# Optimization experiments

Hardware: AMD Instinct MI355X
Metric: run time of the kernel (lower is better)

The kernel has to match this reference:

```python
import jax, jax.numpy as jnp
import numpy as np

D_MODEL = 256
N_HEADS = 8


def setup_inputs() -> dict:
    key = jax.random.key(0)
    ks = jax.random.split(key, 12)
    B, S, d, H = 4, 1024, D_MODEL, N_HEADS
    s = 0.02
    return {
        "Q": jax.random.normal(ks[0], (B, S, d), jnp.float32),
        "K": jax.random.normal(ks[1], (B, S, d), jnp.float32),
        "V": jax.random.normal(ks[2], (B, S, d), jnp.float32),
        "Wq": jax.random.normal(ks[3], (d, d * H), jnp.float32) * s,
        "bq": jnp.zeros((d * H,), jnp.float32),
        "Wk": jax.random.normal(ks[4], (d, d * H), jnp.float32) * s,
        "bk": jnp.zeros((d * H,), jnp.float32),
        "Wv": jax.random.normal(ks[5], (d, d * H), jnp.float32) * s,
        "bv": jnp.zeros((d * H,), jnp.float32),
        "Wo": jax.random.normal(ks[6], (H * d, d), jnp.float32) * s,
        "bo": jnp.zeros((d,), jnp.float32),
    }


def reference(Q, K, V, Wq, bq, Wk, bk, Wv, bv, Wo, bo):
    B, S, d = Q.shape
    H = N_HEADS
    # projections: [B,S,d] -> [B,S,H*d] -> [B,H,S,d] (head_dim == d_model here)
    q = (Q @ Wq + bq).reshape(B, S, H, d).transpose(0, 2, 1, 3)
    k = (K @ Wk + bk).reshape(B, S, H, d).transpose(0, 2, 1, 3)
    v = (V @ Wv + bv).reshape(B, S, H, d).transpose(0, 2, 1, 3)
    scores = jnp.einsum("bhqd,bhkd->bhqk", q, k) / jnp.sqrt(jnp.float32(d))
    attn = jax.nn.softmax(scores, axis=-1)
    out = jnp.einsum("bhqk,bhkd->bhqd", attn, v)  # [B,H,S,d]
    out = out.transpose(0, 2, 1, 3).reshape(B, S, H * d)
    return out @ Wo + bo
```

## Files before the change

kernel.cpp:

```cpp
#include <hip/hip_runtime.h>
#include <stdint.h>

#define NB 4
#define SEQ 1024
#define DM 256
#define NH 8

typedef __attribute__((ext_vector_type(8))) short bf8;
typedef __attribute__((ext_vector_type(4))) float f4;

__device__ __forceinline__ unsigned short f2bf(float f) {
  union { float f; uint32_t u; } c; c.f = f;
  uint32_t u = c.u;
  return (unsigned short)((u + 0x7FFFu + ((u >> 16) & 1u)) >> 16);
}

__device__ __forceinline__ void gl_lds16(const unsigned short* g, short* l) {
  __builtin_amdgcn_global_load_lds(
      (const __attribute__((address_space(1))) unsigned int*)g,
      (__attribute__((address_space(3))) unsigned int*)l, 16, 0, 0);
}


__global__ __launch_bounds__(256) void prep_kernel(
    const float* __restrict__ Wq, const float* __restrict__ Wk,
    const float* __restrict__ Wv, const float* __restrict__ Wo,
    const float* __restrict__ Q, const float* __restrict__ K,
    const float* __restrict__ V,
    unsigned short* __restrict__ Wt3, unsigned short* __restrict__ WoT,
    unsigned short* __restrict__ Xbf) {
  const int z = blockIdx.y;
  const int tid = threadIdx.x;
  if (z >= 4) {
    const float* src = (z == 4) ? Q : (z == 5) ? K : V;
    const size_t off = (size_t)blockIdx.x * 1024 + tid * 4;
    const float4 v = *(const float4*)(src + off);
    short4 s;
    s.x = (short)f2bf(v.x); s.y = (short)f2bf(v.y);
    s.z = (short)f2bf(v.z); s.w = (short)f2bf(v.w);
    *(short4*)(Xbf + (size_t)(z - 4) * 4096 * 256 + off) = s;
    return;
  }
  if (blockIdx.x >= 512) return;
  const float* in;
  unsigned short* out;
  int R, C, bx, by;
  if (z < 3) {
    in = (z == 0) ? Wq : (z == 1) ? Wk : Wv;
    out = Wt3 + (size_t)z * 2048 * 256;
    R = 256; C = 2048; bx = blockIdx.x & 63; by = blockIdx.x >> 6;
  } else {
    in = Wo; out = WoT;
    R = 2048; C = 256; bx = blockIdx.x & 7; by = blockIdx.x >> 3;
  }
  __shared__ float t[32][33];
  const int c0 = bx * 32, r0 = by * 32;
  const int tx = tid & 31, ty = tid >> 5;
#pragma unroll
  for (int i = 0; i < 4; i++) {
    int r = r0 + ty + i * 8;
    t[ty + i * 8][tx] = in[(size_t)r * C + c0 + tx];
  }
  __syncthreads();
#pragma unroll
  for (int i = 0; i < 4; i++) {
    int c = c0 + ty + i * 8;
    out[(size_t)c * R + r0 + tx] = f2bf(t[tx][ty + i * 8]);
  }
}

__global__ __launch_bounds__(256) void proj_kernel(
    const unsigned short* __restrict__ Xbf, const unsigned short* __restrict__ Wt3,
    const float* __restrict__ bq, const float* __restrict__ bk, const float* __restrict__ bv,
    unsigned short* __restrict__ q_frag, unsigned short* __restrict__ k_frag,
    unsigned short* __restrict__ v_frag) {
  const int z = blockIdx.z;
  const unsigned short* X = Xbf + (size_t)z * 4096 * 256;
  const unsigned short* Wt = Wt3 + (size_t)z * 2048 * 256;
  const float* bias = (z == 0) ? bq : (z == 1) ? bk : bv;

  __shared__ short a_lds[128 * 32];
  __shared__ short b_lds[128 * 32];

  const int tid = threadIdx.x;
  const int wid = tid >> 6, lane = tid & 63;
  const int quad = lane >> 4, l16 = lane & 15;
  const int wm = wid >> 1, wn = wid & 1;
  const int m0 = blockIdx.x * 128, n0 = blockIdx.y * 128;

  f4 acc[4][4];
  const f4 z4 = {0.f, 0.f, 0.f, 0.f};
#pragma unroll
  for (int i = 0; i < 4; i++)
#pragma unroll
    for (int j = 0; j < 4; j++) acc[i][j] = z4;

  const int srow = lane >> 2;
  const int schunk = lane & 3;
  const int cxor = quad ^ (l16 & 3);

  for (int ko = 0; ko < 8; ko++) {
    const int k0 = ko * 32;
#pragma unroll
    for (int j = 0; j < 2; j++) {
      const int i = wid * 2 + j;
      const int row = i * 16 + srow;
      const int sc = (schunk ^ (row & 3)) * 8;
      gl_lds16(X + (size_t)(m0 + row) * DM + k0 + sc, a_lds + i * 512);
      gl_lds16(Wt + (size_t)(n0 + row) * DM + k0 + sc, b_lds + i * 512);
    }
    __syncthreads();
    bf8 af[4], bfv[4];
#pragma unroll
    for (int mi = 0; mi < 4; mi++)
      af[mi] = *(const bf8*)(a_lds + (wm * 64 + mi * 16 + l16) * 32 + cxor * 8);
#pragma unroll
    for (int ni = 0; ni < 4; ni++)
      bfv[ni] = *(const bf8*)(b_lds + (wn * 64 + ni * 16 + l16) * 32 + cxor * 8);
    if (z < 2) {
#pragma unroll
      for (int ni = 0; ni < 4; ni++)
#pragma unroll
        for (int mi = 0; mi < 4; mi++)
          acc[ni][mi] = __builtin_amdgcn_mfma_f32_16x16x32_bf16(bfv[ni], af[mi], acc[ni][mi], 0, 0, 0);
    } else {
#pragma unroll
      for (int mi = 0; mi < 4; mi++)
#pragma unroll
        for (int ni = 0; ni < 4; ni++)
          acc[mi][ni] = __builtin_amdgcn_mfma_f32_16x16x32_bf16(af[mi], bfv[ni], acc[mi][ni], 0, 0, 0);
    }
    __syncthreads();
  }

  if (z < 2) {
    const float scale = (z == 0) ? 0.0901684400f : 1.0f;
    unsigned short* dst = (z == 0) ? q_frag : k_frag;
#pragma unroll
    for (int ni = 0; ni < 4; ni++) {
      const int nb = n0 + wn * 64 + ni * 16 + quad * 4;
      const float4 b4 = *(const float4*)(bias + nb);
      const int h = nb >> 8, dd = nb & 255;
      const int dq = (dd >> 3) & 3, jh = dd & 7;
#pragma unroll
      for (int mi = 0; mi < 4; mi++) {
        const int tok = m0 + wm * 64 + mi * 16 + l16;
        const int b = tok >> 10, sr = tok & 1023;
        const size_t idx = ((size_t)(b * NH + h) * 64 + (sr >> 4)) * 4096 +
                           (size_t)(dd >> 5) * 512 + ((sr & 15) + 16 * dq) * 8 + jh;
        short4 s4;
        s4.x = (short)f2bf((acc[ni][mi][0] + b4.x) * scale);
        s4.y = (short)f2bf((acc[ni][mi][1] + b4.y) * scale);
        s4.z = (short)f2bf((acc[ni][mi][2] + b4.z) * scale);
        s4.w = (short)f2bf((acc[ni][mi][3] + b4.w) * scale);
        *(short4*)(dst + idx) = s4;
      }
    }
  } else {
#pragma unroll
    for (int ni = 0; ni < 4; ni++) {
      const int n = n0 + wn * 64 + ni * 16 + l16;
      const float bsv = bias[n];
      const int h = n >> 8, d = n & 255;
#pragma unroll
      for (int mi = 0; mi < 4; mi++) {
        const int m = m0 + wm * 64 + mi * 16 + quad * 4;
        const int b = m >> 10, sr = m & 1023;
        const size_t idx = ((size_t)(b * NH + h) * 16 + (d >> 4)) * 16384 +
                           (size_t)(sr >> 5) * 512 +
                           ((d & 15) + 16 * ((sr >> 3) & 3)) * 8 + (sr & 7);
        short4 s4;
        s4.x = (short)f2bf(acc[mi][ni][0] + bsv);
        s4.y = (short)f2bf(acc[mi][ni][1] + bsv);
        s4.z = (short)f2bf(acc[mi][ni][2] + bsv);
        s4.w = (short)f2bf(acc[mi][ni][3] + bsv);
        *(short4*)(v_frag + idx) = s4;
      }
    }
  }
}

__global__ __launch_bounds__(256, 2) void attn_kernel(
    const unsigned short* __restrict__ q_frag, const unsigned short* __restrict__ k_frag,
    const unsigned short* __restrict__ v_frag, unsigned short* __restrict__ o_ws) {
  __shared__ short k_lds[3 * 8192];
  __shared__ short p_lds[2][2][64][40];
  __shared__ float l_sh[2][64];

  const int tid = threadIdx.x;
  const int wid = tid >> 6, lane = tid & 63;
  const int quad = lane >> 4, l16 = lane & 15;
  const int wq = wid >> 1, wk = wid & 1;
  const int blk = blockIdx.x;
  const int g = blk & 7;
  const int qt = (blk >> 3) & 15;
  const int bh = g + 8 * (blk >> 7);
  const size_t fbase = (size_t)bh * 262144;

  const unsigned short* ksrc = k_frag + fbase + (size_t)wid * 2048 + lane * 8;
#pragma unroll
  for (int jj = 0; jj < 4; jj++) {
    gl_lds16(ksrc + jj * 512, &k_lds[wid * 2048 + jj * 512]);
    gl_lds16(ksrc + 8192 + jj * 512, &k_lds[2 * 8192 + wid * 2048 + jj * 512]);
  }

  bf8 qf[2][8];
#pragma unroll
  for (int qi = 0; qi < 2; qi++) {
    const unsigned short* qp =
        q_frag + fbase + (size_t)(qt * 4 + wq * 2 + qi) * 4096 + lane * 8;
#pragma unroll
    for (int c = 0; c < 8; c++) qf[qi][c] = *(const bf8*)(qp + c * 512);
  }

  const f4 z4 = {0.f, 0.f, 0.f, 0.f};
  f4 Oacc[4][4];
#pragma unroll
  for (int i = 0; i < 4; i++)
#pragma unroll
    for (int j = 0; j < 4; j++) Oacc[i][j] = z4;
  float lpart[2][4] = {{0.f, 0.f, 0.f, 0.f}, {0.f, 0.f, 0.f, 0.f}};

  __syncthreads();

  bf8 vpre[8];
  const unsigned short* vsrc = v_frag + fbase + (size_t)(wid * 4) * 16384 + lane * 8;

  for (int t = 0; t < 16; t++) {
    const int cur = t & 1;
    if (t < 15) {
      const unsigned short* s0 = ksrc + (size_t)(t + 1) * 16384;
#pragma unroll
      for (int jj = 0; jj < 4; jj++)
        gl_lds16(s0 + jj * 512, &k_lds[(cur ^ 1) * 8192 + wid * 2048 + jj * 512]);
    }
    const short* kb_base = &k_lds[(wk ? 2 : cur) * 8192];
    f4 S00 = z4, S01 = z4, S10 = z4, S11 = z4;
#pragma unroll
    for (int c = 0; c < 8; c++) {
      const bf8 kb0 = *(const bf8*)(kb_base + c * 512 + lane * 8);
      const bf8 kb1 = *(const bf8*)(kb_base + 4096 + c * 512 + lane * 8);
      S00 = __builtin_amdgcn_mfma_f32_16x16x32_bf16(qf[0][c], kb0, S00, 0, 0, 0);
      S01 = __builtin_amdgcn_mfma_f32_16x16x32_bf16(qf[0][c], kb1, S01, 0, 0, 0);
      S10 = __builtin_amdgcn_mfma_f32_16x16x32_bf16(qf[1][c], kb0, S10, 0, 0, 0);
      S11 = __builtin_amdgcn_mfma_f32_16x16x32_bf16(qf[1][c], kb1, S11, 0, 0, 0);
    }
    __syncthreads();
    if (t < 15) {
      const unsigned short* s1 = ksrc + (size_t)(t + 1) * 16384 + 8192;
#pragma unroll
      for (int jj = 0; jj < 4; jj++)
        gl_lds16(s1 + jj * 512, &k_lds[2 * 8192 + wid * 2048 + jj * 512]);
    }
    if (t > 0) {
      const int prv = cur ^ 1;
#pragma unroll
      for (int ks = 0; ks < 2; ks++) {
        bf8 pb[4];
#pragma unroll
        for (int nq = 0; nq < 4; nq++)
          pb[nq] = *(const bf8*)(&p_lds[prv][ks][nq * 16 + l16][quad * 8]);
#pragma unroll
        for (int mi = 0; mi < 4; mi++)
#pragma unroll
          for (int nq = 0; nq < 4; nq++)
            Oacc[mi][nq] = __builtin_amdgcn_mfma_f32_16x16x32_bf16(
                vpre[ks * 4 + mi], pb[nq], Oacc[mi][nq], 0, 0, 0);
      }
    }
#pragma unroll
    for (int ks = 0; ks < 2; ks++)
#pragma unroll
      for (int mi = 0; mi < 4; mi++)
        vpre[ks * 4 + mi] =
            *(const bf8*)(vsrc + (size_t)mi * 16384 + (size_t)(2 * t + ks) * 512);
#pragma unroll
    for (int reg = 0; reg < 4; reg++) {
      {
        const int qrow = wq * 32 + quad * 4 + reg;
        const float p0 = exp2f(S00[reg]);
        const float p1 = exp2f(S01[reg]);
        lpart[0][reg] += p0 + p1;
        union { float f; uint32_t u; } c0, c1;
        c0.f = p0; c1.f = p1;
        p_lds[cur][wk][qrow][l16] = (short)((c0.u + 0x8000u) >> 16);
        p_lds[cur][wk][qrow][16 + l16] = (short)((c1.u + 0x8000u) >> 16);
      }
      {
        const int qrow = wq * 32 + 16 + quad * 4 + reg;
        const float p0 = exp2f(S10[reg]);
        const float p1 = exp2f(S11[reg]);
        lpart[1][reg] += p0 + p1;
        union { float f; uint32_t u; } c0, c1;
        c0.f = p0; c1.f = p1;
        p_lds[cur][wk][qrow][l16] = (short)((c0.u + 0x8000u) >> 16);
        p_lds[cur][wk][qrow][16 + l16] = (short)((c1.u + 0x8000u) >> 16);
      }
    }
    __syncthreads();
  }

  {
#pragma unroll
    for (int ks = 0; ks < 2; ks++) {
      bf8 pb[4];
#pragma unroll
      for (int nq = 0; nq < 4; nq++)
        pb[nq] = *(const bf8*)(&p_lds[1][ks][nq * 16 + l16][quad * 8]);
#pragma unroll
      for (int mi = 0; mi < 4; mi++)
#pragma unroll
        for (int nq = 0; nq < 4; nq++)
          Oacc[mi][nq] = __builtin_amdgcn_mfma_f32_16x16x32_bf16(
              vpre[ks * 4 + mi], pb[nq], Oacc[mi][nq], 0, 0, 0);
    }
  }

#pragma unroll
  for (int qi = 0; qi < 2; qi++)
#pragma unroll
    for (int reg = 0; reg < 4; reg++) {
      float v = lpart[qi][reg];
      v += __shfl_xor(v, 1, 64);
      v += __shfl_xor(v, 2, 64);
      v += __shfl_xor(v, 4, 64);
      v += __shfl_xor(v, 8, 64);
      if (l16 == 0) l_sh[wk][wq * 32 + qi * 16 + quad * 4 + reg] = v;
    }
  __syncthreads();

  const int b = bh >> 3, h = bh & 7;
#pragma unroll
  for (int nq = 0; nq < 4; nq++) {
    const int q = nq * 16 + l16;
    const float inv = 1.f / (l_sh[0][q] + l_sh[1][q]);
    const size_t base = ((size_t)b * SEQ + qt * 64 + q) * (NH * DM) + h * DM + wid * 64;
#pragma unroll
    for (int mi = 0; mi < 4; mi++) {
      short4 s4;
      s4.x = (short)f2bf(Oacc[mi][nq][0] * inv);
      s4.y = (short)f2bf(Oacc[mi][nq][1] * inv);
      s4.z = (short)f2bf(Oacc[mi][nq][2] * inv);
      s4.w = (short)f2bf(Oacc[mi][nq][3] * inv);
      *(short4*)(o_ws + base + mi * 16 + quad * 4) = s4;
    }
  }
}

__global__ __launch_bounds__(256) void outproj_kernel(
    const unsigned short* __restrict__ o_ws, const unsigned short* __restrict__ WoT,
    const float* __restrict__ bo, float* __restrict__ out) {
  __shared__ short a_lds[32][136];
  __shared__ short b_lds[64][136];

  const int tid = threadIdx.x;
  const int wid = tid >> 6, lane = tid & 63;
  const int quad = lane >> 4, l16 = lane & 15;
  const int wm = wid & 1, wn = wid >> 1;
  const int m0 = blockIdx.x * 32, n0 = blockIdx.y * 64;

  const f4 z4 = {0.f, 0.f, 0.f, 0.f};
  f4 acc[2];
#pragma unroll
  for (int i = 0; i < 2; i++) acc[i] = z4;

  const int ch = tid & 15, row = tid >> 4;
  for (int ko = 0; ko < 16; ko++) {
    const int k0 = ko * 128;
#pragma unroll
    for (int rb = 0; rb < 2; rb++) {
      int r = row + rb * 16;
      *(bf8*)(&a_lds[r][ch * 8]) = *(const bf8*)(o_ws + (size_t)(m0 + r) * 2048 + k0 + ch * 8);
    }
#pragma unroll
    for (int rb = 0; rb < 4; rb++) {
      int r = row + rb * 16;
      *(bf8*)(&b_lds[r][ch * 8]) = *(const bf8*)(WoT + (size_t)(n0 + r) * 2048 + k0 + ch * 8);
    }
    __syncthreads();
#pragma unroll
    for (int kc = 0; kc < 4; kc++) {
      const bf8 af = *(const bf8*)(&a_lds[wm * 16 + l16][kc * 32 + quad * 8]);
      bf8 bfv[2];
#pragma unroll
      for (int ni = 0; ni < 2; ni++)
        bfv[ni] = *(const bf8*)(&b_lds[wn * 32 + ni * 16 + l16][kc * 32 + quad * 8]);
#pragma unroll
      for (int ni = 0; ni < 2; ni++)
        acc[ni] = __builtin_amdgcn_mfma_f32_16x16x32_bf16(af, bfv[ni], acc[ni], 0, 0, 0);
    }
    __syncthreads();
  }
#pragma unroll
  for (int ni = 0; ni < 2; ni++) {
    const int n = n0 + wn * 32 + ni * 16 + l16;
    const float bv = bo[n];
#pragma unroll
    for (int reg = 0; reg < 4; reg++) {
      const int m = m0 + wm * 16 + quad * 4 + reg;
      out[(size_t)m * DM + n] = acc[ni][reg] + bv;
    }
  }
}

extern "C" void kernel_launch(void* const* d_in, const int* in_sizes, int n_in,
                              void* d_out, int out_size, void* d_ws, size_t ws_size,
                              hipStream_t stream) {
  const float* Q  = (const float*)d_in[0];
  const float* K  = (const float*)d_in[1];
  const float* V  = (const float*)d_in[2];
  const float* Wq = (const float*)d_in[3];
  const float* bq = (const float*)d_in[4];
  const float* Wk = (const float*)d_in[5];
  const float* bk = (const float*)d_in[6];
  const float* Wv = (const float*)d_in[7];
  const float* bv = (const float*)d_in[8];
  const float* Wo = (const float*)d_in[9];
  const float* bo = (const float*)d_in[10];
  float* out = (float*)d_out;

  char* ws = (char*)d_ws;
  const size_t QS = (size_t)NB * NH * SEQ * DM * 2;
  unsigned short* q_frag = (unsigned short*)(ws);
  unsigned short* k_frag = (unsigned short*)(ws + QS);
  unsigned short* v_frag = (unsigned short*)(ws + 2 * QS);
  unsigned short* o_ws   = (unsigned short*)(ws + 3 * QS);
  const size_t WT = (size_t)2048 * 256 * 2;
  unsigned short* Wt3 = (unsigned short*)(ws + 4 * QS);
  unsigned short* WoT = (unsigned short*)(ws + 4 * QS + 3 * WT);
  unsigned short* Xbf = o_ws;

  prep_kernel<<<dim3(1024, 7), 256, 0, stream>>>(Wq, Wk, Wv, Wo, Q, K, V,
                                                 Wt3, WoT, Xbf);
  proj_kernel<<<dim3(32, 16, 3), 256, 0, stream>>>(Xbf, Wt3, bq, bk, bv,
                                                   q_frag, k_frag, v_frag);
  attn_kernel<<<512, 256, 0, stream>>>(q_frag, k_frag, v_frag, o_ws);
  outproj_kernel<<<dim3(128, 4), 256, 0, stream>>>(o_ws, WoT, bo, out);
}
```

Before: 171.0 us.

## Restructure attention loop to 32-key tiles with triple-buffered K prefetch

The attention main loop now processes 32-key tiles in 32 iterations instead of 64-key tiles in 16. Each wave owns 16 query rows across all keys rather than splitting keys between wave pairs, which removes the second row-sum buffer and the split P layout. K tiles rotate through a three-slot LDS ring with a two-ahead prefetch, and the two syncthreads per iteration become one explicit lgkmcnt wait plus barrier, with scheduling fences. The intent is less synchronisation and better overlap of loads with MFMA work. In exchange there are more iterations, each with less MFMA work and smaller register fragments, and the code depends on exact buffer index arithmetic.

Result: no change. 174.0 us (+1.8%).

```diff
diff --git a/kernel.cpp b/kernel.cpp
--- a/kernel.cpp
+++ b/kernel.cpp
@@ -184,33 +184,30 @@
     const unsigned short* __restrict__ q_frag, const unsigned short* __restrict__ k_frag,
     const unsigned short* __restrict__ v_frag, unsigned short* __restrict__ o_ws) {
   __shared__ short k_lds[3 * 8192];
-  __shared__ short p_lds[2][2][64][40];
-  __shared__ float l_sh[2][64];
+  __shared__ short p_lds[2][64][40];
+  __shared__ float l_sh[64];
 
   const int tid = threadIdx.x;
   const int wid = tid >> 6, lane = tid & 63;
   const int quad = lane >> 4, l16 = lane & 15;
-  const int wq = wid >> 1, wk = wid & 1;
   const int blk = blockIdx.x;
   const int g = blk & 7;
   const int qt = (blk >> 3) & 15;
   const int bh = g + 8 * (blk >> 7);
   const size_t fbase = (size_t)bh * 262144;
 
-  const unsigned short* ksrc = k_frag + fbase + (size_t)wid * 2048 + lane * 8;
+  const unsigned short* kdma_src = k_frag + fbase + (size_t)wid * 2048 + lane * 8;
 #pragma unroll
   for (int jj = 0; jj < 4; jj++) {
-    gl_lds16(ksrc + jj * 512, &k_lds[wid * 2048 + jj * 512]);
-    gl_lds16(ksrc + 8192 + jj * 512, &k_lds[2 * 8192 + wid * 2048 + jj * 512]);
-  }
-
-  bf8 qf[2][8];
-#pragma unroll
-  for (int qi = 0; qi < 2; qi++) {
-    const unsigned short* qp =
-        q_frag + fbase + (size_t)(qt * 4 + wq * 2 + qi) * 4096 + lane * 8;
-#pragma unroll
-    for (int c = 0; c < 8; c++) qf[qi][c] = *(const bf8*)(qp + c * 512);
+    gl_lds16(kdma_src + jj * 512, &k_lds[wid * 2048 + jj * 512]);
+    gl_lds16(kdma_src + 8192 + jj * 512, &k_lds[8192 + wid * 2048 + jj * 512]);
+  }
+
+  bf8 qf[8];
+  {
+    const unsigned short* qp = q_frag + fbase + (size_t)(qt * 4 + wid) * 4096 + lane * 8;
+#pragma unroll
+    for (int kc = 0; kc < 8; kc++) qf[kc] = *(const bf8*)(qp + kc * 512);
   }
 
   const f4 z4 = {0.f, 0.f, 0.f, 0.f};
@@ -219,121 +216,112 @@
   for (int i = 0; i < 4; i++)
 #pragma unroll
     for (int j = 0; j < 4; j++) Oacc[i][j] = z4;
-  float lpart[2][4] = {{0.f, 0.f, 0.f, 0.f}, {0.f, 0.f, 0.f, 0.f}};
+  float lpart[4] = {0.f, 0.f, 0.f, 0.f};
 
   __syncthreads();
 
-  bf8 vpre[8];
+  bf8 vpre[4];
   const unsigned short* vsrc = v_frag + fbase + (size_t)(wid * 4) * 16384 + lane * 8;
-
-  for (int t = 0; t < 16; t++) {
-    const int cur = t & 1;
-    if (t < 15) {
-      const unsigned short* s0 = ksrc + (size_t)(t + 1) * 16384;
+  short* const pB = &p_lds[0][0][0];
+
+  int kRd = 0;
+  int kPre = 2 * 8192;
+
+#pragma unroll 1
+  for (int t = 0; t < 32; ++t) {
+    if (t < 30) {
+      const unsigned short* s0 = kdma_src + (size_t)(t + 2) * 8192;
 #pragma unroll
       for (int jj = 0; jj < 4; jj++)
-        gl_lds16(s0 + jj * 512, &k_lds[(cur ^ 1) * 8192 + wid * 2048 + jj * 512]);
-    }
-    const short* kb_base = &k_lds[(wk ? 2 : cur) * 8192];
-    f4 S00 = z4, S01 = z4, S10 = z4, S11 = z4;
-#pragma unroll
-    for (int c = 0; c < 8; c++) {
-      const bf8 kb0 = *(const bf8*)(kb_base + c * 512 + lane * 8);
-      const bf8 kb1 = *(const bf8*)(kb_base + 4096 + c * 512 + lane * 8);
-      S00 = __builtin_amdgcn_mfma_f32_16x16x32_bf16(qf[0][c], kb0, S00, 0, 0, 0);
-      S01 = __builtin_amdgcn_mfma_f32_16x16x32_bf16(qf[0][c], kb1, S01, 0, 0, 0);
-      S10 = __builtin_amdgcn_mfma_f32_16x16x32_bf16(qf[1][c], kb0, S10, 0, 0, 0);
-      S11 = __builtin_amdgcn_mfma_f32_16x16x32_bf16(qf[1][c], kb1, S11, 0, 0, 0);
-    }
-    __syncthreads();
-    if (t < 15) {
-      const unsigned short* s1 = ksrc + (size_t)(t + 1) * 16384 + 8192;
-#pragma unroll
-      for (int jj = 0; jj < 4; jj++)
-        gl_lds16(s1 + jj * 512, &k_lds[2 * 8192 + wid * 2048 + jj * 512]);
-    }
+        gl_lds16(s0 + jj * 512, &k_lds[kPre + wid * 2048 + jj * 512]);
+    }
+    __builtin_amdgcn_sched_barrier(0);
+
+    f4 S0a = z4, S0b = z4, S1a = z4, S1b = z4;
+#pragma unroll
+    for (int cc = 0; cc < 4; cc++) {
+      const bf8 k0a = *(const bf8*)(&k_lds[kRd + (2 * cc) * 512 + lane * 8]);
+      const bf8 k0b = *(const bf8*)(&k_lds[kRd + (2 * cc + 1) * 512 + lane * 8]);
+      const bf8 k1a = *(const bf8*)(&k_lds[kRd + (8 + 2 * cc) * 512 + lane * 8]);
+      const bf8 k1b = *(const bf8*)(&k_lds[kRd + (8 + 2 * cc + 1) * 512 + lane * 8]);
+      S0a = __builtin_amdgcn_mfma_f32_16x16x32_bf16(qf[2 * cc], k0a, S0a, 0, 0, 0);
+      S0b = __builtin_amdgcn_mfma_f32_16x16x32_bf16(qf[2 * cc + 1], k0b, S0b, 0, 0, 0);
+      S1a = __builtin_amdgcn_mfma_f32_16x16x32_bf16(qf[2 * cc], k1a, S1a, 0, 0, 0);
+      S1b = __builtin_amdgcn_mfma_f32_16x16x32_bf16(qf[2 * cc + 1], k1b, S1b, 0, 0, 0);
+    }
+    const f4 S0 = S0a + S0b;
+    const f4 S1 = S1a + S1b;
+
     if (t > 0) {
-      const int prv = cur ^ 1;
-#pragma unroll
-      for (int ks = 0; ks < 2; ks++) {
-        bf8 pb[4];
+      const int pprv = (((t & 1) ^ 1) << 11) + (((t & 1) ^ 1) << 9);
+      bf8 pb[4];
+#pragma unroll
+      for (int nq = 0; nq < 4; nq++)
+        pb[nq] = *(const bf8*)(pB + pprv + (nq * 16 + l16) * 40 + quad * 8);
+#pragma unroll
+      for (int mi = 0; mi < 4; mi++)
 #pragma unroll
         for (int nq = 0; nq < 4; nq++)
-          pb[nq] = *(const bf8*)(&p_lds[prv][ks][nq * 16 + l16][quad * 8]);
-#pragma unroll
-        for (int mi = 0; mi < 4; mi++)
-#pragma unroll
-          for (int nq = 0; nq < 4; nq++)
-            Oacc[mi][nq] = __builtin_amdgcn_mfma_f32_16x16x32_bf16(
-                vpre[ks * 4 + mi], pb[nq], Oacc[mi][nq], 0, 0, 0);
-      }
-    }
-#pragma unroll
-    for (int ks = 0; ks < 2; ks++)
-#pragma unroll
-      for (int mi = 0; mi < 4; mi++)
-        vpre[ks * 4 + mi] =
-            *(const bf8*)(vsrc + (size_t)mi * 16384 + (size_t)(2 * t + ks) * 512);
-#pragma unroll
-    for (int reg = 0; reg < 4; reg++) {
-      {
-        const int qrow = wq * 32 + quad * 4 + reg;
-        const float p0 = exp2f(S00[reg]);
-        const float p1 = exp2f(S01[reg]);
-        lpart[0][reg] += p0 + p1;
+          Oacc[mi][nq] = __builtin_amdgcn_mfma_f32_16x16x32_bf16(
+              vpre[mi], pb[nq], Oacc[mi][nq], 0, 0, 0);
+    }
+
+#pragma unroll
+    for (int mi = 0; mi < 4; mi++)
+      vpre[mi] = *(const bf8*)(vsrc + (size_t)mi * 16384 + (size_t)t * 512);
+
+    {
+      const int pcur = ((t & 1) << 11) + ((t & 1) << 9);
+#pragma unroll
+      for (int reg = 0; reg < 4; reg++) {
+        const int qrow = wid * 16 + quad * 4 + reg;
+        const float p0 = exp2f(S0[reg]);
+        const float p1 = exp2f(S1[reg]);
+        lpart[reg] += p0 + p1;
         union { float f; uint32_t u; } c0, c1;
         c0.f = p0; c1.f = p1;
-        p_lds[cur][wk][qrow][l16] = (short)((c0.u + 0x8000u) >> 16);
-        p_lds[cur][wk][qrow][16 + l16] = (short)((c1.u + 0x8000u) >> 16);
+        pB[pcur + qrow * 40 + l16] = (short)((c0.u + 0x8000u) >> 16);
+        pB[pcur + qrow * 40 + 16 + l16] = (short)((c1.u + 0x8000u) >> 16);
       }
-      {
-        const int qrow = wq * 32 + 16 + quad * 4 + reg;
-        const float p0 = exp2f(S10[reg]);
-        const float p1 = exp2f(S11[reg]);
-        lpart[1][reg] += p0 + p1;
-        union { float f; uint32_t u; } c0, c1;
-        c0.f = p0; c1.f = p1;
-        p_lds[cur][wk][qrow][l16] = (short)((c0.u + 0x8000u) >> 16);
-        p_lds[cur][wk][qrow][16 + l16] = (short)((c1.u + 0x8000u) >> 16);
-      }
-    }
-    __syncthreads();
+    }
+
+    asm volatile("s_waitcnt lgkmcnt(0)" ::: "memory");
+    __builtin_amdgcn_s_barrier();
+    __builtin_amdgcn_sched_barrier(0);
+
+    kRd += 8192;  if (kRd == 24576) kRd = 0;
+    kPre += 8192; if (kPre == 24576) kPre = 0;
   }
 
   {
-#pragma unroll
-    for (int ks = 0; ks < 2; ks++) {
-      bf8 pb[4];
+    bf8 pb[4];
+#pragma unroll
+    for (int nq = 0; nq < 4; nq++)
+      pb[nq] = *(const bf8*)(pB + 2560 + (nq * 16 + l16) * 40 + quad * 8);
+#pragma unroll
+    for (int mi = 0; mi < 4; mi++)
 #pragma unroll
       for (int nq = 0; nq < 4; nq++)
-        pb[nq] = *(const bf8*)(&p_lds[1][ks][nq * 16 + l16][quad * 8]);
-#pragma unroll
-      for (int mi = 0; mi < 4; mi++)
-#pragma unroll
-        for (int nq = 0; nq < 4; nq++)
-          Oacc[mi][nq] = __builtin_amdgcn_mfma_f32_16x16x32_bf16(
-              vpre[ks * 4 + mi], pb[nq], Oacc[mi][nq], 0, 0, 0);
-    }
-  }
-
-#pragma unroll
-  for (int qi = 0; qi < 2; qi++)
-#pragma unroll
-    for (int reg = 0; reg < 4; reg++) {
-      float v = lpart[qi][reg];
-      v += __shfl_xor(v, 1, 64);
-      v += __shfl_xor(v, 2, 64);
-      v += __shfl_xor(v, 4, 64);
-      v += __shfl_xor(v, 8, 64);
-      if (l16 == 0) l_sh[wk][wq * 32 + qi * 16 + quad * 4 + reg] = v;
-    }
+        Oacc[mi][nq] = __builtin_amdgcn_mfma_f32_16x16x32_bf16(
+            vpre[mi], pb[nq], Oacc[mi][nq], 0, 0, 0);
+  }
+
+#pragma unroll
+  for (int reg = 0; reg < 4; reg++) {
+    float v = lpart[reg];
+    v += __shfl_xor(v, 1, 64);
+    v += __shfl_xor(v, 2, 64);
+    v += __shfl_xor(v, 4, 64);
+    v += __shfl_xor(v, 8, 64);
+    if (l16 == 0) l_sh[wid * 16 + quad * 4 + reg] = v;
+  }
   __syncthreads();
 
   const int b = bh >> 3, h = bh & 7;
 #pragma unroll
   for (int nq = 0; nq < 4; nq++) {
     const int q = nq * 16 + l16;
-    const float inv = 1.f / (l_sh[0][q] + l_sh[1][q]);
+    const float inv = 1.f / l_sh[q];
     const size_t base = ((size_t)b * SEQ + qt * 64 + q) * (NH * DM) + h * DM + wid * 64;
 #pragma unroll
     for (int mi = 0; mi < 4; mi++) {
```
